# Kernel tuning notes

Measured on AMD Instinct MI355X. Metric: run time of the kernel, lower is better.

## Reference

```python
import jax, jax.numpy as jnp
import numpy as np

N = 25000      # nodes
E = 300000     # edges
IN = 32        # in_dim
EDF = 16       # edge_feat_dim
HID = 256      # hidden_dim (per-head dim, concat=False)
HEADS = 4
ACT = 16       # num_actions
G = 64         # graphs in batch
KW = 1024      # wire-mask query nodes


def setup_inputs() -> dict:
    key = jax.random.key(0)
    ks = jax.random.split(key, 20)
    def rn(k, shape, s=0.1):
        return jax.random.normal(k, shape, jnp.float32) * s
    return {
        "x": jax.random.normal(ks[0], (N, IN), jnp.float32),
        "edge_attr": jax.random.normal(ks[1], (E, EDF), jnp.float32),
        "wire_mask": jax.random.randint(ks[2], (KW,), 0, N, jnp.int32),
        "edge_index": jax.random.randint(ks[3], (2, E), 0, N, jnp.int32),
        "batch": jnp.sort(jax.random.randint(ks[4], (N,), 0, G, jnp.int32)),
        "enc_w1": rn(ks[5], (EDF, 32)),
        "enc_b1": jnp.zeros((32,), jnp.float32),
        "enc_w2": rn(ks[6], (32, IN * IN), 0.05),
        "enc_b2": jnp.zeros((IN * IN,), jnp.float32),
        "root_w": rn(ks[7], (IN, IN)),
        "nn_bias": jnp.zeros((IN,), jnp.float32),
        "gat1_w": rn(ks[8], (IN, HEADS * HID)),
        "gat1_asrc": rn(ks[9], (HEADS, HID)),
        "gat1_adst": rn(ks[10], (HEADS, HID)),
        "gat1_b": jnp.zeros((HID,), jnp.float32),
        "gat2_w": rn(ks[11], (HID, HEADS * HID)),
        "gat2_asrc": rn(ks[12], (HEADS, HID)),
        "gat2_adst": rn(ks[13], (HEADS, HID)),
        "gat2_b": jnp.zeros((HID,), jnp.float32),
        "wire_w": rn(ks[14], (HID, 1)),
        "wire_b": jnp.zeros((1,), jnp.float32),
        "act_w": rn(ks[15], (HID, ACT)),
        "act_b": jnp.zeros((ACT,), jnp.float32),
    }


def _gat(x, src, dst, W, a_src, a_dst, b):
    # PyG GATConv, concat=False (mean over heads), eval mode (no dropout),
    # self-loops already included in (src, dst).
    H, D = a_src.shape
    h = (x @ W).reshape(-1, H, D)                      # [N, H, D]
    es = (h * a_src[None]).sum(-1)                     # [N, H]
    ed = (h * a_dst[None]).sum(-1)                     # [N, H]
    e = jax.nn.leaky_relu(es[src] + ed[dst], negative_slope=0.2)  # [E2, H]
    m = jax.ops.segment_max(e, dst, num_segments=N)    # segment softmax (stable)
    w = jnp.exp(e - m[dst])
    den = jax.ops.segment_sum(w, dst, num_segments=N)
    alpha = w / (den[dst] + 1e-16)
    out = jax.ops.segment_sum(h[src] * alpha[..., None], dst, num_segments=N)
    return out.mean(axis=1) + b                        # [N, D]


def reference(x, edge_attr, wire_mask, edge_index, batch,
              enc_w1, enc_b1, enc_w2, enc_b2, root_w, nn_bias,
              gat1_w, gat1_asrc, gat1_adst, gat1_b,
              gat2_w, gat2_asrc, gat2_adst, gat2_b,
              wire_w, wire_b, act_w, act_b):
    src, dst = edge_index[0], edge_index[1]
    # NNConv (aggr='mean'): per-edge weight matrix from edge MLP
    We = (jax.nn.relu(edge_attr @ enc_w1 + enc_b1) @ enc_w2 + enc_b2)
    We = We.reshape(E, IN, IN)                         # [E, in, out]
    msg = jnp.einsum('ei,eio->eo', x[src], We)         # [E, out]
    s = jax.ops.segment_sum(msg, dst, num_segments=N)
    cnt = jax.ops.segment_sum(jnp.ones((E,), x.dtype), dst, num_segments=N)
    agg = s / jnp.maximum(cnt, 1.0)[:, None]
    h0 = jax.nn.relu(agg + x @ root_w + nn_bias)
    # GATConv default add_self_loops=True
    sl = jnp.arange(N, dtype=src.dtype)
    src2 = jnp.concatenate([src, sl])
    dst2 = jnp.concatenate([dst, sl])
    h1 = jax.nn.relu(_gat(h0, src2, dst2, gat1_w, gat1_asrc, gat1_adst, gat1_b))
    h2 = jax.nn.relu(_gat(h1, src2, dst2, gat2_w, gat2_asrc, gat2_adst, gat2_b))
    p_wire = (h2[wire_mask] @ wire_w + wire_b).squeeze(-1)   # [KW]
    pooled_s = jax.ops.segment_sum(h2, batch, num_segments=G)
    gc = jax.ops.segment_sum(jnp.ones((N,), h2.dtype), batch, num_segments=G)
    pooled = pooled_s / jnp.maximum(gc, 1.0)[:, None]        # global_mean_pool
    p_action = pooled @ act_w + act_b                        # [G, ACT]
    return (p_wire, p_action)
```

## Files before the change

kernel.cpp:

```cpp
#include <hip/hip_runtime.h>
#include <hip/hip_fp16.h>

#define N_NODES 25000
#define M_PAD   25024
#define N_TILES 1564
#define N_EDGES 300000
#define IN_DIM  32
#define EDFD    16
#define HIDD    256
#define HEADS   4
#define NACT    16
#define NGRAPH  64
#define KWIRE   1024
#define POOL_NB 64

typedef _Float16 half8v __attribute__((ext_vector_type(8)));
typedef __attribute__((ext_vector_type(4))) float f32x4;

__device__ __forceinline__ float leaky(float v) { return v > 0.f ? v : 0.2f * v; }

__global__ __launch_bounds__(256) void k_deg2(const int* __restrict__ ei,
                                              int* __restrict__ deg,
                                              int* __restrict__ deg2) {
    int e = blockIdx.x * 256 + threadIdx.x;
    if (e >= N_EDGES) return;
    atomicAdd(&deg[ei[N_EDGES + e]], 1);
    atomicAdd(&deg2[ei[e]], 1);
}

__global__ __launch_bounds__(256) void k_scan2(const int* __restrict__ degA, int* __restrict__ rpA,
                                               const int* __restrict__ degB, int* __restrict__ rpB) {
    const int* deg = blockIdx.x ? degB : degA;
    int* rowptr    = blockIdx.x ? rpB : rpA;
    __shared__ int part[256];
    int t = threadIdx.x;
    const int CH = 98;
    int base = t * CH;
    int s = 0;
    for (int i = 0; i < CH; ++i) {
        int idx = base + i;
        if (idx < N_NODES) s += deg[idx];
    }
    part[t] = s;
    __syncthreads();
    if (t == 0) {
        int run = 0;
        for (int i = 0; i < 256; ++i) { int v = part[i]; part[i] = run; run += v; }
    }
    __syncthreads();
    int run = part[t];
    for (int i = 0; i < CH; ++i) {
        int idx = base + i;
        if (idx < N_NODES) { rowptr[idx] = run; run += deg[idx]; }
    }
    if (N_NODES >= base && N_NODES < base + CH) rowptr[N_NODES] = run;
}

__global__ __launch_bounds__(256) void k_scatter2(const int* __restrict__ ei,
                                                  const float* __restrict__ ea,
                                                  const int* __restrict__ rowptr,
                                                  const int* __restrict__ rowptr2,
                                                  int* __restrict__ cursor,
                                                  int* __restrict__ cursor2,
                                                  int* __restrict__ csrc,
                                                  int* __restrict__ cdst,
                                                  __half* __restrict__ eaP) {
    int e = blockIdx.x * 256 + threadIdx.x;
    if (e >= N_EDGES) return;
    int src = ei[e], dst = ei[N_EDGES + e];
    int p1 = atomicAdd(&cursor[dst], 1);
    csrc[rowptr[dst] + p1] = src;
    int p2 = atomicAdd(&cursor2[src], 1);
    int r2 = rowptr2[src] + p2;
    cdst[r2] = dst;
    const float4* src4 = (const float4*)(ea + (size_t)e * EDFD);
    __half2* dp = (__half2*)(eaP + (size_t)r2 * EDFD);
    #pragma unroll
    for (int q = 0; q < EDFD / 4; ++q) {
        float4 v = src4[q];
        dp[q * 2]     = __float22half2_rn(make_float2(v.x, v.y));
        dp[q * 2 + 1] = __float22half2_rn(make_float2(v.z, v.w));
    }
}

__global__ __launch_bounds__(256) void k_prep(const float* __restrict__ w2,
                                              const float* __restrict__ W1,
                                              const float* __restrict__ W2,
                                              const float* __restrict__ a1s,
                                              const float* __restrict__ a1d,
                                              const float* __restrict__ a2s,
                                              const float* __restrict__ a2d,
                                              const float* __restrict__ x,
                                              const float* __restrict__ b2,
                                              __half* __restrict__ wtt,
                                              __half* __restrict__ wb1,
                                              __half* __restrict__ wb2,
                                              float* __restrict__ wa1,
                                              float* __restrict__ wd1,
                                              float* __restrict__ wa2,
                                              float* __restrict__ wd2,
                                              __half* __restrict__ xf,
                                              float* __restrict__ xb) {
    int bid = blockIdx.x, t = threadIdx.x;
    if (bid < 128) {
        int idx = bid * 256 + t;
        int co = idx >> 5, i = idx & 31;
        wtt[idx] = __float2half(w2[(co >> 5) * 1024 + i * 32 + (co & 31)]);
    } else if (bid < 256) {
        int idx = (bid - 128) * 256 + t;
        int d = idx >> 7, k = idx & 127;
        int h = k >> 5, i = k & 31;
        wb1[idx] = __float2half(0.25f * W1[i * 1024 + h * 256 + d]);
    } else if (bid < 1280) {
        int idx = (bid - 256) * 256 + t;
        int d = idx >> 10, k = idx & 1023;
        int h = k >> 8, i = k & 255;
        wb2[idx] = __float2half(0.25f * W2[i * 1024 + h * 256 + d]);
    } else if (bid < 4405) {
        int idx = (bid - 1280) * 256 + t;
        if (idx >= N_NODES * 32) return;
        int n = idx >> 5, o = idx & 31;
        xf[idx] = __float2half(x[idx]);
        float s = 0.f;
        for (int i = 0; i < 32; ++i) s += x[n * 32 + i] * b2[i * 32 + o];
        xb[idx] = s;
    } else if (bid == 4405) {
        if (t >= 128) return;
        int h = t >> 5, i = t & 31;
        float s = 0.f, sd = 0.f;
        for (int d = 0; d < 256; ++d) {
            float w = W1[i * 1024 + h * 256 + d];
            s  += w * a1s[h * 256 + d];
            sd += w * a1d[h * 256 + d];
        }
        wa1[t] = s; wd1[t] = sd;
    } else {
        int idx = (bid - 4406) * 256 + t;
        if (idx >= 1024) return;
        int h = idx >> 8, i = idx & 255;
        float s = 0.f, sd = 0.f;
        for (int d = 0; d < 256; ++d) {
            float w = W2[i * 1024 + h * 256 + d];
            s  += w * a2s[h * 256 + d];
            sd += w * a2d[h * 256 + d];
        }
        wa2[idx] = s; wd2[idx] = sd;
    }
}

__global__ __launch_bounds__(256) void k_msg2(const int* __restrict__ rowptr2,
                                              const int* __restrict__ cdst,
                                              const __half* __restrict__ eaP,
                                              const float* __restrict__ w1,
                                              const float* __restrict__ b1,
                                              const __half* __restrict__ T,
                                              const float* __restrict__ xb,
                                              float* __restrict__ agg) {
    int g = threadIdx.x >> 5, o = threadIdx.x & 31;
    int src = blockIdx.x * 8 + g;
    if (src >= N_NODES) return;
    int r0 = rowptr2[src], r1 = rowptr2[src + 1];
    if (r0 == r1) return;
    float tcol[32];
    const __half* Tp = T + (size_t)src * 1024 + o;
    #pragma unroll
    for (int j = 0; j < 32; ++j) tcol[j] = __half2float(Tp[j * 32]);
    float w1col[EDFD];
    #pragma unroll
    for (int k = 0; k < EDFD; ++k) w1col[k] = w1[k * 32 + o];
    float b1o = b1[o];
    float xbv = xb[src * 32 + o];
    for (int r = r0; r < r1; ++r) {
        int dst = cdst[r];
        const __half2* h2p = (const __half2*)(eaP + (size_t)r * EDFD);
        float a = b1o;
        #pragma unroll
        for (int q = 0; q < EDFD / 2; ++q) {
            float2 v = __half22float2(h2p[q]);
            a += v.x * w1col[2 * q] + v.y * w1col[2 * q + 1];
        }
        a = fmaxf(a, 0.f);
        float m = xbv;
        #pragma unroll
        for (int j = 0; j < 32; ++j)
            m += __shfl(a, j, 32) * tcol[j];
        atomicAdd(&agg[dst * 32 + o], m);
    }
}

__global__ __launch_bounds__(256) void k_h0e(const float* __restrict__ x,
                                             const float* __restrict__ root_w,
                                             const float* __restrict__ nn_bias,
                                             const float* __restrict__ agg,
                                             const int* __restrict__ rowptr,
                                             const float* __restrict__ wa,
                                             const float* __restrict__ wd,
                                             __half* __restrict__ h0f,
                                             float* __restrict__ es,
                                             float* __restrict__ ed) {
    int t = threadIdx.x;
    int ng = t >> 5, o = t & 31;
    int n = blockIdx.x * 8 + ng;
    if (n >= N_NODES) return;
    float s = nn_bias[o];
    for (int k = 0; k < IN_DIM; ++k) s += x[n * IN_DIM + k] * root_w[k * 32 + o];
    float c = fmaxf((float)(rowptr[n + 1] - rowptr[n]), 1.f);
    s += agg[n * IN_DIM + o] / c;
    float v = fmaxf(s, 0.f);
    h0f[n * IN_DIM + o] = __float2half(v);
    #pragma unroll
    for (int h = 0; h < 4; ++h) {
        float ss = v * wa[h * 32 + o];
        float dd = v * wd[h * 32 + o];
        #pragma unroll
        for (int off = 16; off; off >>= 1) {
            ss += __shfl_down(ss, off, 32);
            dd += __shfl_down(dd, off, 32);
        }
        if (o == 0) { es[n * 4 + h] = ss; ed[n * 4 + h] = dd; }
    }
}

__global__ __launch_bounds__(256, 2) void k_gemT(const __half* __restrict__ A,
                                                 const __half* __restrict__ Wt,
                                                 __half* __restrict__ C) {
    __shared__ __half cst[4][16 * 36];
    int t = threadIdx.x, wid = t >> 6, lane = t & 63;
    int lr = lane & 15, lk = (lane >> 4) * 8;

    int bid = blockIdx.x;
    int xcd = bid & 7, j = bid >> 3;
    int sx = j & 31;
    int y = ((j >> 5) << 3) | xcd;
    int n0 = sx * 32;

    half8v bfr[2];
    #pragma unroll
    for (int c = 0; c < 2; ++c)
        bfr[c] = *(const half8v*)(Wt + (size_t)(n0 + c * 16 + lr) * 32 + lk);

    int tb = (y * 4 + wid) * 4;
    for (int pp = 0; pp < 4; pp += 2) {
        int tA = tb + pp;
        if (tA >= N_TILES) break;
        int mA = tA * 16, mB = mA + 16;
        half8v aA = *(const half8v*)(A + (size_t)(mA + lr) * 32 + lk);
        half8v aB = *(const half8v*)(A + (size_t)(mB + lr) * 32 + lk);
        f32x4 acc[2][2];
        #pragma unroll
        for (int i = 0; i < 2; ++i)
            #pragma unroll
            for (int c = 0; c < 2; ++c)
                acc[i][c] = (f32x4){0.f, 0.f, 0.f, 0.f};
        acc[0][0] = __builtin_amdgcn_mfma_f32_16x16x32_f16(aA, bfr[0], acc[0][0], 0, 0, 0);
        acc[0][1] = __builtin_amdgcn_mfma_f32_16x16x32_f16(aA, bfr[1], acc[0][1], 0, 0, 0);
        acc[1][0] = __builtin_amdgcn_mfma_f32_16x16x32_f16(aB, bfr[0], acc[1][0], 0, 0, 0);
        acc[1][1] = __builtin_amdgcn_mfma_f32_16x16x32_f16(aB, bfr[1], acc[1][1], 0, 0, 0);

        int rbase = (lane >> 4) * 4;
        #pragma unroll
        for (int ti = 0; ti < 2; ++ti) {
            #pragma unroll
            for (int c = 0; c < 2; ++c)
                #pragma unroll
                for (int r = 0; r < 4; ++r)
                    cst[wid][(rbase + r) * 36 + c * 16 + lr] = __float2half(acc[ti][c][r]);
            int m0 = ti ? mB : mA;
            #pragma unroll
            for (int p = 0; p < 2; ++p) {
                int row = p * 8 + (lane >> 3), hb = lane & 7;
                float2 v = *(const float2*)((const char*)&cst[wid][0] + row * 72 + hb * 8);
                *(float2*)((char*)C + ((size_t)(m0 + row) * 1024 + n0) * 2 + hb * 8) = v;
            }
        }
    }
}

template <int K, typename OT>
__global__ __launch_bounds__(256) void k_gemmo(const __half* __restrict__ A,
                                               const __half* __restrict__ Wt,
                                               const float* __restrict__ bias,
                                               OT* __restrict__ C) {
    constexpr int CK  = 128;
    constexpr int KC  = K / CK;
    constexpr int KSC = CK / 32;
    constexpr int CB  = CK * 2;
    __shared__ __half bs[2][32 * CK];
    __shared__ float cst[4][16 * 36];
    int t = threadIdx.x, wid = t >> 6, lane = t & 63;
    int lr = lane & 15, lk = (lane >> 4) * 8;

    int bid = blockIdx.x;
    int xcd = bid & 7, rest = bid >> 3;
    int strip = rest & 7, yhi = rest >> 3;
    int y = yhi * 8 + xcd;
    if (y >= 98) return;
    int n0 = strip * 32;
    float bv0 = bias[n0 + lr], bv1 = bias[n0 + 16 + lr];
    int tb = (y * 4 + wid) * 4;
    const int swz = (lr & 7) << 4;

    f32x4 acc[2][2][2];
    #pragma unroll
    for (int pi = 0; pi < 2; ++pi)
        #pragma unroll
        for (int i = 0; i < 2; ++i)
            #pragma unroll
            for (int c = 0; c < 2; ++c)
                acc[pi][i][c] = (f32x4){0.f, 0.f, 0.f, 0.f};

    for (int i = t * 16; i < 32 * CB; i += 256 * 16) {
        int col = i / CB, offb = i % CB;
        const char* src = (const char*)Wt + ((size_t)(n0 + col) * K) * 2 + offb;
        *(float4*)((char*)bs[0] + (i ^ ((col & 7) << 4))) = *(const float4*)src;
    }
    __syncthreads();

    for (int kc = 0; kc < KC; ++kc) {
        int cur = kc & 1;
        if (kc + 1 < KC) {
            for (int i = t * 16; i < 32 * CB; i += 256 * 16) {
                int col = i / CB, offb = i % CB;
                const char* src = (const char*)Wt + (((size_t)(n0 + col) * K + (kc + 1) * CK) * 2 + offb);
                *(float4*)((char*)bs[cur ^ 1] + (i ^ ((col & 7) << 4))) = *(const float4*)src;
            }
        }
        #pragma unroll
        for (int pi = 0; pi < 2; ++pi) {
            int tA = tb + pi * 2;
            if (tA >= N_TILES) continue;
            int mA = tA * 16, mB = mA + 16;
            const __half* pA = A + (size_t)(mA + lr) * K + kc * CK + lk;
            const __half* pB = A + (size_t)(mB + lr) * K + kc * CK + lk;
            #pragma unroll
            for (int ks = 0; ks < KSC; ++ks) {
                half8v aA = *(const half8v*)(pA + (size_t)ks * 32);
                half8v aB = *(const half8v*)(pB + (size_t)ks * 32);
                half8v b0 = *(const half8v*)((const char*)bs[cur] + ((( 0 + lr) * CB + lk * 2 + ks * 64) ^ swz));
                half8v b1 = *(const half8v*)((const char*)bs[cur] + (((16 + lr) * CB + lk * 2 + ks * 64) ^ swz));
                acc[pi][0][0] = __builtin_amdgcn_mfma_f32_16x16x32_f16(aA, b0, acc[pi][0][0], 0, 0, 0);
                acc[pi][0][1] = __builtin_amdgcn_mfma_f32_16x16x32_f16(aA, b1, acc[pi][0][1], 0, 0, 0);
                acc[pi][1][0] = __builtin_amdgcn_mfma_f32_16x16x32_f16(aB, b0, acc[pi][1][0], 0, 0, 0);
                acc[pi][1][1] = __builtin_amdgcn_mfma_f32_16x16x32_f16(aB, b1, acc[pi][1][1], 0, 0, 0);
            }
        }
        if (kc + 1 < KC) __syncthreads();
    }

    int rbase = (lane >> 4) * 4;
    #pragma unroll
    for (int pi = 0; pi < 2; ++pi) {
        int tA = tb + pi * 2;
        if (tA >= N_TILES) continue;
        #pragma unroll
        for (int ti = 0; ti < 2; ++ti) {
            #pragma unroll
            for (int c = 0; c < 2; ++c)
                #pragma unroll
                for (int r = 0; r < 4; ++r)
                    cst[wid][(rbase + r) * 36 + c * 16 + lr] =
                        fmaxf(acc[pi][ti][c][r] + (c ? bv1 : bv0), 0.f);
            int m0 = tA * 16 + ti * 16;
            int row = lane >> 2, cg = lane & 3;
            const float* sp = &cst[wid][row * 36 + cg * 8];
            if constexpr (sizeof(OT) == 2) {
                __half2 o0 = __float22half2_rn(make_float2(sp[0], sp[1]));
                __half2 o1 = __float22half2_rn(make_float2(sp[2], sp[3]));
                __half2 o2 = __float22half2_rn(make_float2(sp[4], sp[5]));
                __half2 o3 = __float22half2_rn(make_float2(sp[6], sp[7]));
                float4 v = make_float4(__uint_as_float(*(unsigned*)&o0), __uint_as_float(*(unsigned*)&o1),
                                       __uint_as_float(*(unsigned*)&o2), __uint_as_float(*(unsigned*)&o3));
                *(float4*)((__half*)C + (size_t)(m0 + row) * 256 + n0 + cg * 8) = v;
            } else {
                float4 v0 = make_float4(sp[0], sp[1], sp[2], sp[3]);
                float4 v1 = make_float4(sp[4], sp[5], sp[6], sp[7]);
                float* cp = (float*)C + (size_t)(m0 + row) * 256 + n0 + cg * 8;
                *(float4*)cp = v0;
                *(float4*)(cp + 4) = v1;
            }
        }
    }
}

__global__ __launch_bounds__(256) void k_esed2(const __half* __restrict__ h1f,
                                               const float* __restrict__ wa,
                                               const float* __restrict__ wd,
                                               float* __restrict__ es,
                                               float* __restrict__ ed) {
    int n = blockIdx.x;
    int h = threadIdx.x >> 6, lane = threadIdx.x & 63;
    float s = 0.f, d2 = 0.f;
    for (int d = lane; d < 256; d += 64) {
        float v = __half2float(h1f[(size_t)n * 256 + d]);
        s  += v * wa[h * 256 + d];
        d2 += v * wd[h * 256 + d];
    }
    #pragma unroll
    for (int off = 32; off; off >>= 1) {
        s  += __shfl_down(s, off);
        d2 += __shfl_down(d2, off);
    }
    if (lane == 0) { es[n * 4 + h] = s; ed[n * 4 + h] = d2; }
}

__global__ __launch_bounds__(256) void k_agg1(const int* __restrict__ rowptr,
                                              const int* __restrict__ csrc,
                                              const float* __restrict__ es,
                                              const float* __restrict__ ed,
                                              const __half* __restrict__ h0f,
                                              __half* __restrict__ agg0) {
    int dst = blockIdx.x * 4 + (threadIdx.x >> 6);
    if (dst >= N_NODES) return;
    int lane = threadIdx.x & 63;
    int h = lane >> 4, i2 = lane & 15;
    float edv = ed[dst * 4 + h];
    float vself = leaky(es[dst * 4 + h] + edv);
    float dn = 1.f;
    int r0 = rowptr[dst], r1 = rowptr[dst + 1];

    __half2 hv = *(const __half2*)(h0f + (size_t)dst * 32 + i2 * 2);
    float2 f = __half22float2(hv);
    float ax = f.x, ay = f.y;
    for (int r = r0; r < r1; ++r) {
        int src = csrc[r];
        float w = __expf(leaky(es[src * 4 + h] + edv) - vself);
        dn += w;
        __half2 sv = *(const __half2*)(h0f + (size_t)src * 32 + i2 * 2);
        float2 g = __half22float2(sv);
        ax += w * g.x; ay += w * g.y;
    }
    float inv = 1.f / (dn + 1e-16f);
    *(__half2*)(agg0 + (size_t)dst * 128 + h * 32 + i2 * 2) =
        __float22half2_rn(make_float2(ax * inv, ay * inv));
}

__global__ __launch_bounds__(256) void k_agg2(const int* __restrict__ rowptr,
                                              const int* __restrict__ csrc,
                                              const float* __restrict__ es,
                                              const float* __restrict__ ed,
                                              const __half* __restrict__ h1f,
                                              __half* __restrict__ agg1) {
    int dst = blockIdx.x * 4 + (threadIdx.x >> 6);
    if (dst >= N_NODES) return;
    int lane = threadIdx.x & 63;
    float vs[4], edv[4], dn[4];
    float acc[4][4];
    {
        float2 q = *(const float2*)(h1f + (size_t)dst * 256 + lane * 4);
        const __half2* hq = (const __half2*)&q;
        float2 f0 = __half22float2(hq[0]), f1 = __half22float2(hq[1]);
        #pragma unroll
        for (int h = 0; h < 4; ++h) {
            edv[h] = ed[dst * 4 + h];
            vs[h] = leaky(es[dst * 4 + h] + edv[h]);
            dn[h] = 1.f;
            acc[h][0] = f0.x; acc[h][1] = f0.y;
            acc[h][2] = f1.x; acc[h][3] = f1.y;
        }
    }
    int r0 = rowptr[dst], r1 = rowptr[dst + 1];
    for (int r = r0; r < r1; ++r) {
        int src = csrc[r];
        float4 esv = *(const float4*)(es + (size_t)src * 4);
        float w0 = __expf(leaky(esv.x + edv[0]) - vs[0]);
        float w1 = __expf(leaky(esv.y + edv[1]) - vs[1]);
        float w2 = __expf(leaky(esv.z + edv[2]) - vs[2]);
        float w3 = __expf(leaky(esv.w + edv[3]) - vs[3]);
        dn[0] += w0; dn[1] += w1; dn[2] += w2; dn[3] += w3;
        float2 q = *(const float2*)(h1f + (size_t)src * 256 + lane * 4);
        const __half2* hq = (const __half2*)&q;
        float2 f0 = __half22float2(hq[0]), f1 = __half22float2(hq[1]);
        acc[0][0] += w0 * f0.x; acc[0][1] += w0 * f0.y; acc[0][2] += w0 * f1.x; acc[0][3] += w0 * f1.y;
        acc[1][0] += w1 * f0.x; acc[1][1] += w1 * f0.y; acc[1][2] += w1 * f1.x; acc[1][3] += w1 * f1.y;
        acc[2][0] += w2 * f0.x; acc[2][1] += w2 * f0.y; acc[2][2] += w2 * f1.x; acc[2][3] += w2 * f1.y;
        acc[3][0] += w3 * f0.x; acc[3][1] += w3 * f0.y; acc[3][2] += w3 * f1.x; acc[3][3] += w3 * f1.y;
    }
    #pragma unroll
    for (int h = 0; h < 4; ++h) {
        float inv = 1.f / (dn[h] + 1e-16f);
        __half2 o0 = __float22half2_rn(make_float2(acc[h][0] * inv, acc[h][1] * inv));
        __half2 o1 = __float22half2_rn(make_float2(acc[h][2] * inv, acc[h][3] * inv));
        __half2* op = (__half2*)(agg1 + (size_t)dst * 1024 + h * 256 + lane * 4);
        op[0] = o0; op[1] = o1;
    }
}

__global__ __launch_bounds__(256) void k_wirepool(const int* __restrict__ wm,
                                                  const float* __restrict__ h2,
                                                  const float* __restrict__ ww,
                                                  const float* __restrict__ wb,
                                                  const int* __restrict__ batch,
                                                  float* __restrict__ out,
                                                  float* __restrict__ pooled,
                                                  float* __restrict__ gcnt) {
    int bid = blockIdx.x;
    if (bid < KWIRE / 4) {
        int k = bid * 4 + (threadIdx.x >> 6);
        int lane = threadIdx.x & 63;
        int n = wm[k];
        float s = 0.f;
        for (int d = lane; d < 256; d += 64) s += h2[(size_t)n * 256 + d] * ww[d];
        #pragma unroll
        for (int off = 32; off; off >>= 1) s += __shfl_down(s, off);
        if (lane == 0) out[k] = s + wb[0];
        return;
    }
    int n0 = (bid - KWIRE / 4) * POOL_NB;
    int n1 = n0 + POOL_NB; if (n1 > N_NODES) n1 = N_NODES;
    int d = threadIdx.x;
    int cur = batch[n0];
    float acc = 0.f, cnt = 0.f;
    for (int n = n0; n < n1; ++n) {
        int g = batch[n];
        if (g != cur) {
            atomicAdd(&pooled[cur * 256 + d], acc);
            if (d == 0) atomicAdd(&gcnt[cur], cnt);
            acc = 0.f; cnt = 0.f; cur = g;
        }
        acc += h2[(size_t)n * 256 + d];
        cnt += 1.f;
    }
    atomicAdd(&pooled[cur * 256 + d], acc);
    if (d == 0) atomicAdd(&gcnt[cur], cnt);
}

__global__ __launch_bounds__(256) void k_act(const float* __restrict__ pooled,
                                             const float* __restrict__ gcnt,
                                             const float* __restrict__ aw,
                                             const float* __restrict__ ab,
                                             float* __restrict__ out) {
    int u = blockIdx.x * 4 + (threadIdx.x >> 6);
    int lane = threadIdx.x & 63;
    if (u >= NGRAPH * NACT) return;
    int g = u >> 4, a = u & 15;
    float c = fmaxf(gcnt[g], 1.f);
    float s = 0.f;
    for (int d = lane; d < 256; d += 64) s += pooled[g * 256 + d] * aw[d * 16 + a];
    #pragma unroll
    for (int off = 32; off; off >>= 1) s += __shfl_down(s, off);
    if (lane == 0) out[KWIRE + u] = s / c + ab[a];
}

extern "C" void kernel_launch(void* const* d_in, const int* in_sizes, int n_in,
                              void* d_out, int out_size, void* d_ws, size_t ws_size,
                              hipStream_t stream) {
    const float* x        = (const float*)d_in[0];
    const float* edge_attr= (const float*)d_in[1];
    const int*   wire_mask= (const int*)d_in[2];
    const int*   edge_idx = (const int*)d_in[3];
    const int*   batch    = (const int*)d_in[4];
    const float* enc_w1   = (const float*)d_in[5];
    const float* enc_b1   = (const float*)d_in[6];
    const float* enc_w2   = (const float*)d_in[7];
    const float* enc_b2   = (const float*)d_in[8];
    const float* root_w   = (const float*)d_in[9];
    const float* nn_bias  = (const float*)d_in[10];
    const float* gat1_w   = (const float*)d_in[11];
    const float* gat1_asrc= (const float*)d_in[12];
    const float* gat1_adst= (const float*)d_in[13];
    const float* gat1_b   = (const float*)d_in[14];
    const float* gat2_w   = (const float*)d_in[15];
    const float* gat2_asrc= (const float*)d_in[16];
    const float* gat2_adst= (const float*)d_in[17];
    const float* gat2_b   = (const float*)d_in[18];
    const float* wire_w   = (const float*)d_in[19];
    const float* wire_b   = (const float*)d_in[20];
    const float* act_w    = (const float*)d_in[21];
    const float* act_b    = (const float*)d_in[22];
    float* out = (float*)d_out;

    float* ws = (float*)d_ws;
    size_t off = 0;
    __half* T16   = (__half*)(ws + off); off += (size_t)M_PAD * 1024 / 2;
    __half* agg1f = (__half*)(ws + off); off += (size_t)M_PAD * 1024 / 2;
    __half* agg0f = (__half*)(ws + off); off += (size_t)M_PAD * 128 / 2;
    __half* h0f   = (__half*)(ws + off); off += (size_t)M_PAD * 32 / 2;
    __half* h1f   = (__half*)(ws + off); off += (size_t)M_PAD * 256 / 2;
    __half* xf    = (__half*)(ws + off); off += (size_t)M_PAD * 32 / 2;
    __half* eaP   = (__half*)(ws + off); off += (size_t)N_EDGES * EDFD / 2;
    float* xb     = ws + off; off += 800000;
    float* agg    = ws + off; off += 800000;
    float* esb    = ws + off; off += 100000;
    float* edb    = ws + off; off += 100000;
    float* h2     = ws + off; off += (size_t)M_PAD * 256;
    float* pooled = ws + off; off += NGRAPH * 256;
    float* gcnt   = ws + off; off += NGRAPH;
    int* deg      = (int*)(ws + off); off += 25600;
    int* deg2     = (int*)(ws + off); off += 25600;
    int* cursor   = (int*)(ws + off); off += 25600;
    int* cursor2  = (int*)(ws + off); off += 25600;
    int* rowptr   = (int*)(ws + off); off += 25600;
    int* rowptr2  = (int*)(ws + off); off += 25600;
    int* csrc     = (int*)(ws + off); off += N_EDGES;
    int* cdst     = (int*)(ws + off); off += N_EDGES;
    __half* wtt   = (__half*)(ws + off); off += 16384;
    __half* wb1t  = (__half*)(ws + off); off += 16384;
    __half* wb2t  = (__half*)(ws + off); off += 131072;
    float* wa1    = ws + off; off += 128;
    float* wd1    = ws + off; off += 128;
    float* wa2    = ws + off; off += 1024;
    float* wd2    = ws + off; off += 1024;

    const int GBT = 3328;
    const int GBO = 832;

    hipMemsetAsync(deg, 0, 4 * 25600 * sizeof(int), stream);
    k_deg2<<<(N_EDGES + 255) / 256, 256, 0, stream>>>(edge_idx, deg, deg2);
    k_scan2<<<2, 256, 0, stream>>>(deg, rowptr, deg2, rowptr2);
    k_scatter2<<<(N_EDGES + 255) / 256, 256, 0, stream>>>(edge_idx, edge_attr, rowptr, rowptr2,
                                                          cursor, cursor2, csrc, cdst, eaP);

    k_prep<<<4410, 256, 0, stream>>>(enc_w2, gat1_w, gat2_w, gat1_asrc, gat1_adst,
                                     gat2_asrc, gat2_adst, x, enc_b2,
                                     wtt, wb1t, wb2t, wa1, wd1, wa2, wd2, xf, xb);

    hipMemsetAsync(agg, 0, 800000 * sizeof(float), stream);
    k_gemT<<<GBT, 256, 0, stream>>>(xf, wtt, T16);
    k_msg2<<<(N_NODES + 7) / 8, 256, 0, stream>>>(rowptr2, cdst, eaP,
                                                  enc_w1, enc_b1, T16, xb, agg);
    k_h0e<<<(N_NODES + 7) / 8, 256, 0, stream>>>(x, root_w, nn_bias, agg, rowptr,
                                                 wa1, wd1, h0f, esb, edb);

    k_agg1<<<(N_NODES + 3) / 4, 256, 0, stream>>>(rowptr, csrc, esb, edb, h0f, agg0f);
    k_gemmo<128, __half><<<GBO, 256, 0, stream>>>(agg0f, wb1t, gat1_b, h1f);
    k_esed2<<<N_NODES, 256, 0, stream>>>(h1f, wa2, wd2, esb, edb);

    k_agg2<<<(N_NODES + 3) / 4, 256, 0, stream>>>(rowptr, csrc, esb, edb, h1f, agg1f);
    k_gemmo<1024, float><<<GBO, 256, 0, stream>>>(agg1f, wb2t, gat2_b, h2);

    hipMemsetAsync(pooled, 0, (NGRAPH * 256 + NGRAPH) * sizeof(float), stream);
    k_wirepool<<<KWIRE / 4 + (N_NODES + POOL_NB - 1) / POOL_NB, 256, 0, stream>>>(
        wire_mask, h2, wire_w, wire_b, batch, out, pooled, gcnt);
    k_act<<<NGRAPH * NACT / 4, 256, 0, stream>>>(pooled, gcnt, act_w, act_b, out);
}
```

Baseline: 444.5 us.

## Replace atomic edge-message scatter with per-edge buffer and CSR gather

The NNConv message kernel no longer atomically adds each edge message into a per-destination accumulator. It writes fp16 messages into a per-edge buffer, placed through a source-to-destination CSR position map built during scatter. The node kernel then sums its incoming messages by walking its destination CSR range, which also removes the agg memset. The dot product is split across four independent accumulators. The trade is removing atomic contention in exchange for writing and reading a 300k x 32 fp16 buffer, plus fp16 rounding of each message.

```diff
diff --git a/kernel.cpp b/kernel.cpp
--- a/kernel.cpp
+++ b/kernel.cpp
@@ -64,15 +64,18 @@
                                                   int* __restrict__ cursor2,
                                                   int* __restrict__ csrc,
                                                   int* __restrict__ cdst,
+                                                  int* __restrict__ posMap,
                                                   __half* __restrict__ eaP) {
     int e = blockIdx.x * 256 + threadIdx.x;
     if (e >= N_EDGES) return;
     int src = ei[e], dst = ei[N_EDGES + e];
     int p1 = atomicAdd(&cursor[dst], 1);
-    csrc[rowptr[dst] + p1] = src;
+    int r1 = rowptr[dst] + p1;
+    csrc[r1] = src;
     int p2 = atomicAdd(&cursor2[src], 1);
     int r2 = rowptr2[src] + p2;
     cdst[r2] = dst;
+    posMap[r2] = r1;
     const float4* src4 = (const float4*)(ea + (size_t)e * EDFD);
     __half2* dp = (__half2*)(eaP + (size_t)r2 * EDFD);
     #pragma unroll
@@ -149,13 +152,13 @@
 }
 
 __global__ __launch_bounds__(256) void k_msg2(const int* __restrict__ rowptr2,
-                                              const int* __restrict__ cdst,
+                                              const int* __restrict__ posMap,
                                               const __half* __restrict__ eaP,
                                               const float* __restrict__ w1,
                                               const float* __restrict__ b1,
                                               const __half* __restrict__ T,
                                               const float* __restrict__ xb,
-                                              float* __restrict__ agg) {
+                                              __half* __restrict__ msgE) {
     int g = threadIdx.x >> 5, o = threadIdx.x & 31;
     int src = blockIdx.x * 8 + g;
     if (src >= N_NODES) return;
@@ -171,7 +174,7 @@
     float b1o = b1[o];
     float xbv = xb[src * 32 + o];
     for (int r = r0; r < r1; ++r) {
-        int dst = cdst[r];
+        int pm = posMap[r];
         const __half2* h2p = (const __half2*)(eaP + (size_t)r * EDFD);
         float a = b1o;
         #pragma unroll
@@ -180,18 +183,23 @@
             a += v.x * w1col[2 * q] + v.y * w1col[2 * q + 1];
         }
         a = fmaxf(a, 0.f);
-        float m = xbv;
-        #pragma unroll
-        for (int j = 0; j < 32; ++j)
-            m += __shfl(a, j, 32) * tcol[j];
-        atomicAdd(&agg[dst * 32 + o], m);
+        float m0 = 0.f, m1 = 0.f, m2 = 0.f, m3 = 0.f;
+        #pragma unroll
+        for (int j = 0; j < 32; j += 4) {
+            m0 += __shfl(a, j,     32) * tcol[j];
+            m1 += __shfl(a, j + 1, 32) * tcol[j + 1];
+            m2 += __shfl(a, j + 2, 32) * tcol[j + 2];
+            m3 += __shfl(a, j + 3, 32) * tcol[j + 3];
+        }
+        float m = xbv + ((m0 + m1) + (m2 + m3));
+        msgE[(size_t)pm * 32 + o] = __float2half(m);
     }
 }
 
 __global__ __launch_bounds__(256) void k_h0e(const float* __restrict__ x,
                                              const float* __restrict__ root_w,
                                              const float* __restrict__ nn_bias,
-                                             const float* __restrict__ agg,
+                                             const __half* __restrict__ msgE,
                                              const int* __restrict__ rowptr,
                                              const float* __restrict__ wa,
                                              const float* __restrict__ wd,
@@ -204,8 +212,12 @@
     if (n >= N_NODES) return;
     float s = nn_bias[o];
     for (int k = 0; k < IN_DIM; ++k) s += x[n * IN_DIM + k] * root_w[k * 32 + o];
-    float c = fmaxf((float)(rowptr[n + 1] - rowptr[n]), 1.f);
-    s += agg[n * IN_DIM + o] / c;
+    int r0 = rowptr[n], r1 = rowptr[n + 1];
+    float aggv = 0.f;
+    for (int r = r0; r < r1; ++r)
+        aggv += __half2float(msgE[(size_t)r * 32 + o]);
+    float c = fmaxf((float)(r1 - r0), 1.f);
+    s += aggv / c;
     float v = fmaxf(s, 0.f);
     h0f[n * IN_DIM + o] = __float2half(v);
     #pragma unroll
@@ -578,8 +590,8 @@
     __half* h1f   = (__half*)(ws + off); off += (size_t)M_PAD * 256 / 2;
     __half* xf    = (__half*)(ws + off); off += (size_t)M_PAD * 32 / 2;
     __half* eaP   = (__half*)(ws + off); off += (size_t)N_EDGES * EDFD / 2;
+    __half* msgE  = (__half*)(ws + off); off += (size_t)N_EDGES * 32 / 2;
     float* xb     = ws + off; off += 800000;
-    float* agg    = ws + off; off += 800000;
     float* esb    = ws + off; off += 100000;
     float* edb    = ws + off; off += 100000;
     float* h2     = ws + off; off += (size_t)M_PAD * 256;
@@ -593,6 +605,7 @@
     int* rowptr2  = (int*)(ws + off); off += 25600;
     int* csrc     = (int*)(ws + off); off += N_EDGES;
     int* cdst     = (int*)(ws + off); off += N_EDGES;
+    int* posMap   = (int*)(ws + off); off += N_EDGES;
     __half* wtt   = (__half*)(ws + off); off += 16384;
     __half* wb1t  = (__half*)(ws + off); off += 16384;
     __half* wb2t  = (__half*)(ws + off); off += 131072;
@@ -608,17 +621,16 @@
     k_deg2<<<(N_EDGES + 255) / 256, 256, 0, stream>>>(edge_idx, deg, deg2);
     k_scan2<<<2, 256, 0, stream>>>(deg, rowptr, deg2, rowptr2);
     k_scatter2<<<(N_EDGES + 255) / 256, 256, 0, stream>>>(edge_idx, edge_attr, rowptr, rowptr2,
-                                                          cursor, cursor2, csrc, cdst, eaP);
+                                                          cursor, cursor2, csrc, cdst, posMap, eaP);
 
     k_prep<<<4410, 256, 0, stream>>>(enc_w2, gat1_w, gat2_w, gat1_asrc, gat1_adst,
                                      gat2_asrc, gat2_adst, x, enc_b2,
                                      wtt, wb1t, wb2t, wa1, wd1, wa2, wd2, xf, xb);
 
-    hipMemsetAsync(agg, 0, 800000 * sizeof(float), stream);
     k_gemT<<<GBT, 256, 0, stream>>>(xf, wtt, T16);
-    k_msg2<<<(N_NODES + 7) / 8, 256, 0, stream>>>(rowptr2, cdst, eaP,
-                                                  enc_w1, enc_b1, T16, xb, agg);
-    k_h0e<<<(N_NODES + 7) / 8, 256, 0, stream>>>(x, root_w, nn_bias, agg, rowptr,
+    k_msg2<<<(N_NODES + 7) / 8, 256, 0, stream>>>(rowptr2, posMap, eaP,
+                                                  enc_w1, enc_b1, T16, xb, msgE);
+    k_h0e<<<(N_NODES + 7) / 8, 256, 0, stream>>>(x, root_w, nn_bias, msgE, rowptr,
                                                  wa1, wd1, h0f, esb, edb);
 
     k_agg1<<<(N_NODES + 3) / 4, 256, 0, stream>>>(rowptr, csrc, esb, edb, h0f, agg0f);
```

Result: slower. 453.5 us (+2.0%).
